# Kernel tuning notes

Measured on AMD Instinct MI355X. Metric: run time of the kernel, lower is better.

The kernel has to match this reference:

```python
import jax, jax.numpy as jnp
import numpy as np

D_MODEL = 1024
N_HEADS = 16
D_HEAD = D_MODEL // N_HEADS
D_FF = 4 * D_MODEL
EPS = 1e-5


def _layernorm(x, g, b):
    mu = jnp.mean(x, axis=-1, keepdims=True)
    var = jnp.var(x, axis=-1, keepdims=True)
    return (x - mu) * jax.lax.rsqrt(var + EPS) * g + b


def setup_inputs() -> dict:
    key = jax.random.key(0)
    ks = jax.random.split(key, 16)
    s_attn = 1.0 / np.sqrt(D_MODEL)
    s_ff1 = 1.0 / np.sqrt(D_MODEL)
    s_ff2 = 1.0 / np.sqrt(D_FF)
    inp = {
        'x': jax.random.normal(ks[0], (2, 2048, D_MODEL), dtype=jnp.float32),
        'Wq': jax.random.uniform(ks[1], (D_MODEL, D_MODEL), jnp.float32, -s_attn, s_attn),
        'bq': jax.random.uniform(ks[2], (D_MODEL,), jnp.float32, -s_attn, s_attn),
        'Wk': jax.random.uniform(ks[3], (D_MODEL, D_MODEL), jnp.float32, -s_attn, s_attn),
        'bk': jax.random.uniform(ks[4], (D_MODEL,), jnp.float32, -s_attn, s_attn),
        'Wv': jax.random.uniform(ks[5], (D_MODEL, D_MODEL), jnp.float32, -s_attn, s_attn),
        'bv': jax.random.uniform(ks[6], (D_MODEL,), jnp.float32, -s_attn, s_attn),
        'Wo': jax.random.uniform(ks[7], (D_MODEL, D_MODEL), jnp.float32, -s_attn, s_attn),
        'bo': jax.random.uniform(ks[8], (D_MODEL,), jnp.float32, -s_attn, s_attn),
        'W1': jax.random.uniform(ks[9], (D_MODEL, D_FF), jnp.float32, -s_ff1, s_ff1),
        'b1': jax.random.uniform(ks[10], (D_FF,), jnp.float32, -s_ff1, s_ff1),
        'W2': jax.random.uniform(ks[11], (D_FF, D_MODEL), jnp.float32, -s_ff2, s_ff2),
        'b2': jax.random.uniform(ks[12], (D_MODEL,), jnp.float32, -s_ff2, s_ff2),
        'ln1_g': jnp.ones((D_MODEL,), jnp.float32),
        'ln1_b': jnp.zeros((D_MODEL,), jnp.float32),
        'ln2_g': jnp.ones((D_MODEL,), jnp.float32),
        'ln2_b': jnp.zeros((D_MODEL,), jnp.float32),
    }
    return inp


def reference(x, Wq, bq, Wk, bk, Wv, bv, Wo, bo, W1, b1, W2, b2, ln1_g, ln1_b, ln2_g, ln2_b):
    B, T, D = x.shape
    scale = D_HEAD ** -0.5

    # pre-norm MHSA + residual
    h = _layernorm(x, ln1_g, ln1_b)
    def split(z):  # [B,T,D] -> [B,H,T,d_h]
        return z.reshape(B, T, N_HEADS, D_HEAD).transpose(0, 2, 1, 3)
    Q = split(h @ Wq + bq)
    K = split(h @ Wk + bk)
    V = split(h @ Wv + bv)
    scores = jnp.einsum('bhqd,bhkd->bhqk', Q, K) * scale  # [B,H,T,T]
    attn = jax.nn.softmax(scores, axis=-1)
    out = jnp.einsum('bhqk,bhkd->bhqd', attn, V)
    out = out.transpose(0, 2, 1, 3).reshape(B, T, D)
    x = x + (out @ Wo + bo)

    # pre-norm FFN + residual
    h = _layernorm(x, ln2_g, ln2_b)
    ff = jax.nn.gelu(h @ W1 + b1, approximate=False) @ W2 + b2
    return x + ff
```

## Files before the change

### kernel.cpp

```cpp
#include <hip/hip_runtime.h>
#include <math.h>

#define SEQ   2048
#define DM    1024
#define LDQKV 3072
#define MTOK  4096

typedef float  f32x4   __attribute__((ext_vector_type(4)));
typedef __bf16 bf16x8  __attribute__((ext_vector_type(8)));
typedef short  short8  __attribute__((ext_vector_type(8)));
typedef short  short4v __attribute__((ext_vector_type(4)));

__device__ __forceinline__ short f2bf(float f) {
  union { float f; unsigned u; } v; v.f = f;
  unsigned r = v.u + 0x7fffu + ((v.u >> 16) & 1u);
  return (short)(r >> 16);
}

__device__ __forceinline__ void gl_lds16(const void* g, void* l) {
  __builtin_amdgcn_global_load_lds(
      (const __attribute__((address_space(1))) void*)g,
      (__attribute__((address_space(3))) void*)l, 16, 0, 0);
}

__device__ __forceinline__ f32x4 mfma_bf16(bf16x8 a, bf16x8 b, f32x4 c) {
  return __builtin_amdgcn_mfma_f32_16x16x32_bf16(a, b, c, 0, 0, 0);
}

__global__ __launch_bounds__(256) void transpose_cast64_k(
    const float* __restrict__ W, short* __restrict__ Wt, int K, int N)
{
  __shared__ float tile[64][65];
  const int n0 = blockIdx.x * 64, k0 = blockIdx.y * 64;
  const int tid = threadIdx.x;
  const int lr = tid >> 4, lc = (tid & 15) * 4;
#pragma unroll
  for (int i = 0; i < 4; i++) {
    const float4 v = *(const float4*)&W[(size_t)(k0 + lr + i * 16) * N + n0 + lc];
    tile[lr + i * 16][lc]     = v.x;
    tile[lr + i * 16][lc + 1] = v.y;
    tile[lr + i * 16][lc + 2] = v.z;
    tile[lr + i * 16][lc + 3] = v.w;
  }
  __syncthreads();
  const int nr = tid >> 3, ks = (tid & 7) * 8;
#pragma unroll
  for (int i = 0; i < 2; i++) {
    short8 o;
#pragma unroll
    for (int j = 0; j < 8; j++) o[j] = f2bf(tile[ks + j][nr + i * 32]);
    *(short8*)&Wt[(size_t)(n0 + nr + i * 32) * K + k0 + ks] = o;
  }
}

__global__ __launch_bounds__(256) void ln_k(
    const float* __restrict__ x, const float* __restrict__ g,
    const float* __restrict__ b, short* __restrict__ out)
{
  const int row = blockIdx.x;
  const int tid = threadIdx.x;
  const float4 v = ((const float4*)(x + (size_t)row * DM))[tid];
  float s  = v.x + v.y + v.z + v.w;
  float ss = v.x * v.x + v.y * v.y + v.z * v.z + v.w * v.w;
#pragma unroll
  for (int m = 32; m >= 1; m >>= 1) { s += __shfl_xor(s, m); ss += __shfl_xor(ss, m); }
  __shared__ float red[8];
  const int wid = tid >> 6;
  if ((tid & 63) == 0) { red[wid] = s; red[4 + wid] = ss; }
  __syncthreads();
  s  = red[0] + red[1] + red[2] + red[3];
  ss = red[4] + red[5] + red[6] + red[7];
  const float mu  = s * (1.f / DM);
  const float var = ss * (1.f / DM) - mu * mu;
  const float rs  = rsqrtf(var + 1e-5f);
  const float4 gv = ((const float4*)g)[tid];
  const float4 bv = ((const float4*)b)[tid];
  short4v o;
  o[0] = f2bf((v.x - mu) * rs * gv.x + bv.x);
  o[1] = f2bf((v.y - mu) * rs * gv.y + bv.y);
  o[2] = f2bf((v.z - mu) * rs * gv.z + bv.z);
  o[3] = f2bf((v.w - mu) * rs * gv.w + bv.w);
  *(short4v*)(out + (size_t)row * DM + tid * 4) = o;
}

__global__ __launch_bounds__(256) void concat_bias_k(
    const float* __restrict__ bq, const float* __restrict__ bk,
    const float* __restrict__ bv, float* __restrict__ o)
{
  int i = blockIdx.x * 256 + threadIdx.x;
  if (i < 3072) {
    float v = (i < 1024) ? bq[i] : (i < 2048 ? bk[i - 1024] : bv[i - 2048]);
    o[i] = v;
  }
}

__global__ __launch_bounds__(256) void vtrans_k(
    const short* __restrict__ V, short* __restrict__ Vt)
{
  const int b = blockIdx.z, h = blockIdx.y, t0 = blockIdx.x * 64;
  __shared__ short tile[64][72];
  const int tid = threadIdx.x;
  const int r = tid >> 2, c = (tid & 3) * 16;
  const short* src = V + (size_t)(b * SEQ + t0 + r) * LDQKV + h * 64 + c;
  *(short8*)&tile[r][c]     = *(const short8*)src;
  *(short8*)&tile[r][c + 8] = *(const short8*)(src + 8);
  __syncthreads();
  const int d = tid >> 2;
  short8 o0, o1;
#pragma unroll
  for (int k = 0; k < 8; k++) o0[k] = tile[c + k][d];
#pragma unroll
  for (int k = 0; k < 8; k++) o1[k] = tile[c + 8 + k][d];
  short* dst = Vt + (((size_t)(b * 16 + h) * 64) + d) * 2048 + t0 + c;
  *(short8*)dst       = o0;
  *(short8*)(dst + 8) = o1;
}

template <bool GELU_, bool RESID, bool OUTBF16>
__global__ __launch_bounds__(512) void gemm256(
    const short* __restrict__ A, const short* __restrict__ Bt,
    const float* __restrict__ bias, const float* __restrict__ resid,
    void* __restrict__ Cout, int M, int N, int K)
{
  __shared__ __align__(16) short Atile[2][256 * 64];
  __shared__ __align__(16) short Btile[2][256 * 64];

  const int tid = threadIdx.x, lane = tid & 63, wid = tid >> 6;
  const int wm = wid >> 2, wn = wid & 3;

  const int nbn = N >> 8;
  const int chunk = gridDim.x >> 3;
  const int swz = (blockIdx.x & 7) * chunk + (blockIdx.x >> 3);
  const int bm = (swz / nbn) * 256;
  const int bn = (swz % nbn) * 256;

  f32x4 acc[8][4] = {};

  const int srow  = wid * 8 + (lane >> 3);
  const int sslot = (lane & 7) ^ ((lane >> 3) & 7);
  const short* Asrc = A  + (size_t)(bm + srow) * K + sslot * 8;
  const short* Bsrc = Bt + (size_t)(bn + srow) * K + sslot * 8;

#define STAGE256(buf, k0)                                                     \
  {                                                                           \
    _Pragma("unroll")                                                         \
    for (int j = 0; j < 4; j++) {                                             \
      gl_lds16(Asrc + (size_t)(j * 64) * K + (k0), &Atile[buf][(j * 64 + wid * 8) * 64]); \
      gl_lds16(Bsrc + (size_t)(j * 64) * K + (k0), &Btile[buf][(j * 64 + wid * 8) * 64]); \
    }                                                                         \
  }

  const int aRowBase = (wm * 128 + (lane & 15)) * 128;
  const int bRowBase = (wn * 64  + (lane & 15)) * 128;
  const int slot0 = (((lane >> 4)    ) ^ (lane & 7)) * 16;
  const int slot1 = (((lane >> 4) + 4) ^ (lane & 7)) * 16;

#define COMPUTE256(buf)                                                       \
  {                                                                           \
    const char* Ab_ = (const char*)&Atile[buf][0];                            \
    const char* Bb_ = (const char*)&Btile[buf][0];                            \
    _Pragma("unroll")                                                         \
    for (int ks = 0; ks < 2; ks++) {                                          \
      const int sl = ks ? slot1 : slot0;                                      \
      bf16x8 a[8], b[4];                                                      \
      _Pragma("unroll")                                                       \
      for (int mi = 0; mi < 8; mi++)                                          \
        a[mi] = *(const bf16x8*)(Ab_ + aRowBase + mi * 2048 + sl);            \
      _Pragma("unroll")                                                       \
      for (int ni = 0; ni < 4; ni++)                                          \
        b[ni] = *(const bf16x8*)(Bb_ + bRowBase + ni * 2048 + sl);            \
      __builtin_amdgcn_s_setprio(1);                                          \
      _Pragma("unroll")                                                       \
      for (int mi = 0; mi < 8; mi++)                                          \
        _Pragma("unroll")                                                     \
        for (int ni = 0; ni < 4; ni++)                                        \
          acc[mi][ni] = mfma_bf16(a[mi], b[ni], acc[mi][ni]);                 \
      __builtin_amdgcn_s_setprio(0);                                          \
    }                                                                         \
  }

  STAGE256(0, 0);
  __syncthreads();

  int cur = 0;
  const int ntiles = K >> 6;
  for (int t = 1; t < ntiles; ++t) {
    STAGE256(cur ^ 1, t * 64);
    COMPUTE256(cur);
    __syncthreads();
    cur ^= 1;
  }
  COMPUTE256(cur);

#pragma unroll
  for (int mi = 0; mi < 8; mi++) {
#pragma unroll
    for (int ni = 0; ni < 4; ni++) {
      const int col = bn + wn * 64 + ni * 16 + (lane & 15);
      const float bs = bias[col];
#pragma unroll
      for (int j = 0; j < 4; j++) {
        const int row = bm + wm * 128 + mi * 16 + (lane >> 4) * 4 + j;
        float v = acc[mi][ni][j] + bs;
        if (GELU_) v = 0.5f * v * (1.0f + erff(v * 0.70710678118654752f));
        if (RESID) v += resid[(size_t)row * N + col];
        if (OUTBF16) ((short*)Cout)[(size_t)row * N + col] = f2bf(v);
        else         ((float*)Cout)[(size_t)row * N + col] = v;
      }
    }
  }
#undef STAGE256
#undef COMPUTE256
}

template <bool GELU_, bool RESID, bool OUTBF16>
__global__ __launch_bounds__(512) void gemm_bt8(
    const short* __restrict__ A, const short* __restrict__ Bt,
    const float* __restrict__ bias, const float* __restrict__ resid,
    void* __restrict__ Cout, int M, int N, int K)
{
  __shared__ __align__(16) short Ab[2][2][128 * 32];
  __shared__ __align__(16) short Bb[2][2][64 * 32];
  const int tid = threadIdx.x, lane = tid & 63, wid = tid >> 6;
  const int kg = wid >> 2, w2 = wid & 3;
  const int wr = w2 >> 1, wc = w2 & 1;
  const int bm = blockIdx.x * 128, bn = blockIdx.y * 64;

  f32x4 acc[4][2] = {};

  const int r_l = lane >> 2;
  const int c8  = ((lane & 3) ^ ((lane >> 2) & 3)) * 8;
  const short* Ag0 = A  + (size_t)(bm + w2 * 32 + r_l)      * K + c8;
  const short* Ag1 = A  + (size_t)(bm + w2 * 32 + 16 + r_l) * K + c8;
  const short* Bg0 = Bt + (size_t)(bn + w2 * 16 + r_l)      * K + c8;

  const int la0 = (w2 * 32) * 32, la1 = (w2 * 32 + 16) * 32, lb0 = (w2 * 16) * 32;
  const int kbase = kg * 32;
  const int rslot = ((lane >> 4) ^ (lane & 3)) * 8;

  gl_lds16(Ag0 + kbase, &Ab[kg][0][la0]);
  gl_lds16(Ag1 + kbase, &Ab[kg][0][la1]);
  gl_lds16(Bg0 + kbase, &Bb[kg][0][lb0]);
  __syncthreads();

  const int nsteps = K >> 6;
  int cur = 0;
  for (int i = 1; i < nsteps; ++i) {
    const int k0 = i * 64 + kbase;
    const int nxt = cur ^ 1;
    gl_lds16(Ag0 + k0, &Ab[kg][nxt][la0]);
    gl_lds16(Ag1 + k0, &Ab[kg][nxt][la1]);
    gl_lds16(Bg0 + k0, &Bb[kg][nxt][lb0]);

    bf16x8 a[4], b[2];
#pragma unroll
    for (int mi = 0; mi < 4; mi++)
      a[mi] = *(const bf16x8*)&Ab[kg][cur][(wr * 64 + mi * 16 + (lane & 15)) * 32 + rslot];
#pragma unroll
    for (int ni = 0; ni < 2; ni++)
      b[ni] = *(const bf16x8*)&Bb[kg][cur][(wc * 32 + ni * 16 + (lane & 15)) * 32 + rslot];
#pragma unroll
    for (int mi = 0; mi < 4; mi++)
#pragma unroll
      for (int ni = 0; ni < 2; ni++)
        acc[mi][ni] = mfma_bf16(a[mi], b[ni], acc[mi][ni]);

    __syncthreads();
    cur = nxt;
  }

  {
    bf16x8 a[4], b[2];
#pragma unroll
    for (int mi = 0; mi < 4; mi++)
      a[mi] = *(const bf16x8*)&Ab[kg][cur][(wr * 64 + mi * 16 + (lane & 15)) * 32 + rslot];
#pragma unroll
    for (int ni = 0; ni < 2; ni++)
      b[ni] = *(const bf16x8*)&Bb[kg][cur][(wc * 32 + ni * 16 + (lane & 15)) * 32 + rslot];
#pragma unroll
    for (int mi = 0; mi < 4; mi++)
#pragma unroll
      for (int ni = 0; ni < 2; ni++)
        acc[mi][ni] = mfma_bf16(a[mi], b[ni], acc[mi][ni]);
  }

  __syncthreads();

  float* red = (float*)&Ab[0][0][0];
  const int slot = (w2 * 64 + lane) * 8;
  if (kg == 1) {
#pragma unroll
    for (int mi = 0; mi < 4; mi++)
#pragma unroll
      for (int ni = 0; ni < 2; ni++)
        *(f32x4*)&red[(slot + mi * 2 + ni) * 4] = acc[mi][ni];
  }
  __syncthreads();
  if (kg == 0) {
#pragma unroll
    for (int mi = 0; mi < 4; mi++)
#pragma unroll
      for (int ni = 0; ni < 2; ni++)
        acc[mi][ni] += *(const f32x4*)&red[(slot + mi * 2 + ni) * 4];

#pragma unroll
    for (int mi = 0; mi < 4; mi++) {
#pragma unroll
      for (int ni = 0; ni < 2; ni++) {
        const int col = bn + wc * 32 + ni * 16 + (lane & 15);
        const float bs = bias[col];
#pragma unroll
        for (int j = 0; j < 4; j++) {
          const int row = bm + wr * 64 + mi * 16 + (lane >> 4) * 4 + j;
          float v = acc[mi][ni][j] + bs;
          if (GELU_) v = 0.5f * v * (1.0f + erff(v * 0.70710678118654752f));
          if (RESID) v += resid[(size_t)row * N + col];
          if (OUTBF16) ((short*)Cout)[(size_t)row * N + col] = f2bf(v);
          else         ((float*)Cout)[(size_t)row * N + col] = v;
        }
      }
    }
  }
}

__global__ __launch_bounds__(512, 4) void attn_k(
    const short* __restrict__ Qg, const short* __restrict__ Kg,
    const short* __restrict__ Vt, short* __restrict__ Og)
{
  const int phys = blockIdx.x;
  const int lg = (phys & 7) * 64 + (phys >> 3);
  const int q0 = (lg & 15) * 128;
  const int h  = (lg >> 4) & 15;
  const int b  = lg >> 8;

  const int tid = threadIdx.x, lane = tid & 63, w = tid >> 6;
  const int qlane = lane & 15, g = lane >> 4;

  __shared__ __align__(16) short Kl[2][128 * 64];
  __shared__ __align__(16) short Vl[2][64 * 128];

  const size_t qrow = (size_t)(b * SEQ + q0 + w * 16 + qlane) * LDQKV + h * 64;
  const bf16x8 qf0 = *(const bf16x8*)&Qg[qrow + g * 8];
  const bf16x8 qf1 = *(const bf16x8*)&Qg[qrow + 32 + g * 8];

  const int kslot = (lane & 7) ^ ((lane >> 3) & 7);
  const short* Kg_a[2];
#pragma unroll
  for (int i = 0; i < 2; i++) {
    const int r  = i * 64 + w * 8 + (lane >> 3);
    const int kc = r >> 4, gr = (r >> 2) & 3, jr = r & 3;
    const int a  = 32 * (kc & 3) + 8 * gr + 4 * (kc >> 2) + jr;
    Kg_a[i] = Kg + ((size_t)(b * SEQ) + a) * LDQKV + h * 64 + kslot * 8;
  }
  const short* Vg_s[2];
#pragma unroll
  for (int i = 0; i < 2; i++) {
    const int d  = i * 32 + w * 4 + (lane >> 4);
    const int vs = (lane & 15) ^ (d & 15);
    Vg_s[i] = Vt + ((size_t)(b * 16 + h) * 64 + d) * 2048 + vs * 8;
  }

  float m_run = -1e30f, l_run = 0.f;
  f32x4 oacc[4] = {};
  const float C = 0.125f * 1.44269504088896f;

#pragma unroll
  for (int i = 0; i < 2; i++) {
    gl_lds16(Kg_a[i], &Kl[0][(i * 64 + w * 8) * 64]);
    gl_lds16(Vg_s[i], &Vl[0][(i * 32 + w * 4) * 128]);
  }
  __syncthreads();

  int cur = 0;
  for (int kt = 0; kt < SEQ; kt += 128) {
    const int nxt = cur ^ 1;
    if (kt + 128 < SEQ) {
#pragma unroll
      for (int i = 0; i < 2; i++) {
        gl_lds16(Kg_a[i] + (size_t)(kt + 128) * LDQKV, &Kl[nxt][(i * 64 + w * 8) * 64]);
        gl_lds16(Vg_s[i] + (kt + 128),                 &Vl[nxt][(i * 32 + w * 4) * 128]);
      }
    }
    const char* KbC = (const char*)&Kl[cur][0];
    const char* VbC = (const char*)&Vl[cur][0];

    f32x4 s[8];
#pragma unroll
    for (int kc = 0; kc < 8; kc++) {
      const int kr = kc * 16 + qlane;
      const char* kp = KbC + kr * 128;
      const int sw = (kr & 7) << 4;
      bf16x8 kf0 = *(const bf16x8*)(kp + ((g * 16) ^ sw));
      bf16x8 kf1 = *(const bf16x8*)(kp + ((64 + g * 16) ^ sw));
      f32x4 z = {};
      z = mfma_bf16(kf0, qf0, z);
      z = mfma_bf16(kf1, qf1, z);
      s[kc] = z;
    }

    f32x4 m4 = s[0];
#pragma unroll
    for (int kc = 1; kc < 8; kc++) {
      m4[0] = fmaxf(m4[0], s[kc][0]); m4[1] = fmaxf(m4[1], s[kc][1]);
      m4[2] = fmaxf(m4[2], s[kc][2]); m4[3] = fmaxf(m4[3], s[kc][3]);
    }
    float mt = fmaxf(fmaxf(m4[0], m4[1]), fmaxf(m4[2], m4[3]));
    mt = fmaxf(mt, __shfl_xor(mt, 16));
    mt = fmaxf(mt, __shfl_xor(mt, 32));

    if (!__all(mt - m_run <= 40.0f)) {
      const float mnew = fmaxf(m_run, mt);
      const float r = exp2f((m_run - mnew) * C);
      m_run = mnew;
      l_run *= r;
#pragma unroll
      for (int j = 0; j < 4; j++) {
        const float rj = __shfl(r, g * 4 + j);
#pragma unroll
        for (int dt = 0; dt < 4; dt++) oacc[dt][j] *= rj;
      }
    }

    const float nmc = -m_run * C;
    float rs = 0.f;
    unsigned pw[4][4];
#pragma unroll
    for (int kc = 0; kc < 8; kc++) {
      f32x4 p;
#pragma unroll
      for (int j = 0; j < 4; j++) p[j] = exp2f(fmaf(s[kc][j], C, nmc));
      rs += (p[0] + p[1]) + (p[2] + p[3]);
      unsigned w0, w1;
      asm("v_cvt_pk_bf16_f32 %0, %1, %2" : "=v"(w0) : "v"(p[0]), "v"(p[1]));
      asm("v_cvt_pk_bf16_f32 %0, %1, %2" : "=v"(w1) : "v"(p[2]), "v"(p[3]));
      pw[kc & 3][2 * (kc >> 2) + 0] = w0;
      pw[kc & 3][2 * (kc >> 2) + 1] = w1;
    }
    rs += __shfl_xor(rs, 16);
    rs += __shfl_xor(rs, 32);
    l_run += rs;

#pragma unroll
    for (int ks = 0; ks < 4; ks++) {
      union { unsigned u[4]; bf16x8 v; } pf;
      pf.u[0] = pw[ks][0]; pf.u[1] = pw[ks][1];
      pf.u[2] = pw[ks][2]; pf.u[3] = pw[ks][3];
#pragma unroll
      for (int dt = 0; dt < 4; dt++) {
        const int vr = dt * 16 + qlane;
        bf16x8 vf = *(const bf16x8*)(VbC + vr * 256 + ((64 * ks + 16 * g) ^ ((vr & 15) << 4)));
        oacc[dt] = mfma_bf16(pf.v, vf, oacc[dt]);
      }
    }

    __syncthreads();
    cur = nxt;
  }

  const float linv = 1.f / l_run;
#pragma unroll
  for (int j = 0; j < 4; j++) {
    const float lj = __shfl(linv, g * 4 + j);
    const int tok = q0 + w * 16 + g * 4 + j;
#pragma unroll
    for (int dt = 0; dt < 4; dt++)
      Og[(size_t)(b * SEQ + tok) * DM + h * 64 + dt * 16 + qlane] = f2bf(oacc[dt][j] * lj);
  }
}

extern "C" void kernel_launch(void* const* d_in, const int* in_sizes, int n_in,
                              void* d_out, int out_size, void* d_ws, size_t ws_size,
                              hipStream_t stream)
{
  const float* x    = (const float*)d_in[0];
  const float* Wq   = (const float*)d_in[1];
  const float* bq   = (const float*)d_in[2];
  const float* Wk   = (const float*)d_in[3];
  const float* bk   = (const float*)d_in[4];
  const float* Wv   = (const float*)d_in[5];
  const float* bv   = (const float*)d_in[6];
  const float* Wo   = (const float*)d_in[7];
  const float* bo   = (const float*)d_in[8];
  const float* W1   = (const float*)d_in[9];
  const float* b1   = (const float*)d_in[10];
  const float* W2   = (const float*)d_in[11];
  const float* b2   = (const float*)d_in[12];
  const float* ln1g = (const float*)d_in[13];
  const float* ln1b = (const float*)d_in[14];
  const float* ln2g = (const float*)d_in[15];
  const float* ln2b = (const float*)d_in[16];

  char* ws = (char*)d_ws;
  const size_t MB = 1024 * 1024;
  short* Wqkvt = (short*)(ws + 0 * MB);
  short* Wqt   = Wqkvt;
  short* Wkt   = (short*)(ws + 2 * MB);
  short* Wvt   = (short*)(ws + 4 * MB);
  short* Wot   = (short*)(ws + 6 * MB);
  short* W1t   = (short*)(ws + 8 * MB);
  short* W2t   = (short*)(ws + 16 * MB);
  short* hbuf  = (short*)(ws + 24 * MB);
  short* QKV   = (short*)(ws + 32 * MB);
  short* AO    = (short*)(ws + 56 * MB);
  float* x1    = (float*)(ws + 64 * MB);
  short* Vtb   = (short*)(ws + 64 * MB);
  float* bqkv  = (float*)(ws + 80 * MB);
  short* gbuf  = (short*)(ws + 32 * MB);

  dim3 tb(256);

  transpose_cast64_k<<<dim3(16, 16), tb, 0, stream>>>(Wq, Wqt, 1024, 1024);
  transpose_cast64_k<<<dim3(16, 16), tb, 0, stream>>>(Wk, Wkt, 1024, 1024);
  transpose_cast64_k<<<dim3(16, 16), tb, 0, stream>>>(Wv, Wvt, 1024, 1024);
  transpose_cast64_k<<<dim3(16, 16), tb, 0, stream>>>(Wo, Wot, 1024, 1024);
  transpose_cast64_k<<<dim3(64, 16), tb, 0, stream>>>(W1, W1t, 1024, 4096);
  transpose_cast64_k<<<dim3(16, 64), tb, 0, stream>>>(W2, W2t, 4096, 1024);
  concat_bias_k<<<dim3(12), tb, 0, stream>>>(bq, bk, bv, bqkv);

  ln_k<<<dim3(MTOK), tb, 0, stream>>>(x, ln1g, ln1b, hbuf);

  gemm256<false, false, true><<<dim3(192), dim3(512), 0, stream>>>(
      hbuf, Wqkvt, bqkv, nullptr, QKV, MTOK, 3072, 1024);

  vtrans_k<<<dim3(32, 16, 2), tb, 0, stream>>>(QKV + 2048, Vtb);

  attn_k<<<dim3(512), dim3(512), 0, stream>>>(QKV, QKV + 1024, Vtb, AO);

  gemm_bt8<false, true, false><<<dim3(32, 16), dim3(512), 0, stream>>>(
      AO, Wot, bo, x, x1, MTOK, 1024, 1024);

  ln_k<<<dim3(MTOK), tb, 0, stream>>>(x1, ln2g, ln2b, hbuf);

  gemm256<true, false, true><<<dim3(256), dim3(512), 0, stream>>>(
      hbuf, W1t, b1, nullptr, gbuf, MTOK, 4096, 1024);

  gemm_bt8<false, true, false><<<dim3(32, 16), dim3(512), 0, stream>>>(
      gbuf, W2t, b2, x1, (float*)d_out, MTOK, 1024, 4096);
}
```

Measured before the change: 272.4 us.

## Triple-buffer GEMM K-loop with partial vmcnt waits and reswizzled LDS layout

Both GEMM kernels move from double-buffered LDS staging with full __syncthreads to a three-stage ring. Each loop iteration now waits with s_waitcnt vmcnt only for the oldest outstanding tile, so two tiles of global-to-LDS loads stay in flight during compute. The 256x256 kernel also halves its K-tile to 32, which changes the swizzle and staging pattern and roughly halves its LDS footprint. The gain sought is better overlap of memory latency; the cost is twice as many barriers per K in gemm256 and added LDS use in gemm_bt8, which may reduce occupancy.

```diff
diff --git a/kernel.cpp b/kernel.cpp
--- a/kernel.cpp
+++ b/kernel.cpp
@@ -122,8 +122,8 @@
     const float* __restrict__ bias, const float* __restrict__ resid,
     void* __restrict__ Cout, int M, int N, int K)
 {
-  __shared__ __align__(16) short Atile[2][256 * 64];
-  __shared__ __align__(16) short Btile[2][256 * 64];
+  __shared__ __align__(16) short Atile[3][256 * 32];
+  __shared__ __align__(16) short Btile[3][256 * 32];
 
   const int tid = threadIdx.x, lane = tid & 63, wid = tid >> 6;
   const int wm = wid >> 2, wn = wid & 3;
@@ -136,61 +136,61 @@
 
   f32x4 acc[8][4] = {};
 
-  const int srow  = wid * 8 + (lane >> 3);
-  const int sslot = (lane & 7) ^ ((lane >> 3) & 7);
-  const short* Asrc = A  + (size_t)(bm + srow) * K + sslot * 8;
-  const short* Bsrc = Bt + (size_t)(bn + srow) * K + sslot * 8;
+  const int srow = tid >> 2;
+  const int scol = ((tid & 3) ^ ((srow >> 1) & 3)) * 8;
+  const short* Asrc = A  + (size_t)(bm + srow) * K + scol;
+  const short* Bsrc = Bt + (size_t)(bn + srow) * K + scol;
+  const int dst0 = (wid * 16) * 32, dst1 = (128 + wid * 16) * 32;
 
 #define STAGE256(buf, k0)                                                     \
   {                                                                           \
-    _Pragma("unroll")                                                         \
-    for (int j = 0; j < 4; j++) {                                             \
-      gl_lds16(Asrc + (size_t)(j * 64) * K + (k0), &Atile[buf][(j * 64 + wid * 8) * 64]); \
-      gl_lds16(Bsrc + (size_t)(j * 64) * K + (k0), &Btile[buf][(j * 64 + wid * 8) * 64]); \
-    }                                                                         \
-  }
-
-  const int aRowBase = (wm * 128 + (lane & 15)) * 128;
-  const int bRowBase = (wn * 64  + (lane & 15)) * 128;
-  const int slot0 = (((lane >> 4)    ) ^ (lane & 7)) * 16;
-  const int slot1 = (((lane >> 4) + 4) ^ (lane & 7)) * 16;
+    gl_lds16(Asrc + (k0),                   &Atile[buf][dst0]);               \
+    gl_lds16(Asrc + (size_t)128 * K + (k0), &Atile[buf][dst1]);               \
+    gl_lds16(Bsrc + (k0),                   &Btile[buf][dst0]);               \
+    gl_lds16(Bsrc + (size_t)128 * K + (k0), &Btile[buf][dst1]);               \
+  }
+
+  const int rrow  = lane & 15;
+  const int rslot = (((lane >> 4) ^ ((rrow >> 1) & 3))) * 8;
+  const int aOff  = (wm * 128 + rrow) * 32 + rslot;
+  const int bOff  = (wn * 64  + rrow) * 32 + rslot;
 
 #define COMPUTE256(buf)                                                       \
   {                                                                           \
-    const char* Ab_ = (const char*)&Atile[buf][0];                            \
-    const char* Bb_ = (const char*)&Btile[buf][0];                            \
+    const short* Ab_ = &Atile[buf][0];                                        \
+    const short* Bb_ = &Btile[buf][0];                                        \
+    bf16x8 a[8], b[4];                                                        \
     _Pragma("unroll")                                                         \
-    for (int ks = 0; ks < 2; ks++) {                                          \
-      const int sl = ks ? slot1 : slot0;                                      \
-      bf16x8 a[8], b[4];                                                      \
-      _Pragma("unroll")                                                       \
-      for (int mi = 0; mi < 8; mi++)                                          \
-        a[mi] = *(const bf16x8*)(Ab_ + aRowBase + mi * 2048 + sl);            \
+    for (int mi = 0; mi < 8; mi++)                                            \
+      a[mi] = *(const bf16x8*)(Ab_ + aOff + mi * 512);                        \
+    _Pragma("unroll")                                                         \
+    for (int ni = 0; ni < 4; ni++)                                            \
+      b[ni] = *(const bf16x8*)(Bb_ + bOff + ni * 512);                        \
+    __builtin_amdgcn_s_setprio(1);                                            \
+    _Pragma("unroll")                                                         \
+    for (int mi = 0; mi < 8; mi++)                                            \
       _Pragma("unroll")                                                       \
       for (int ni = 0; ni < 4; ni++)                                          \
-        b[ni] = *(const bf16x8*)(Bb_ + bRowBase + ni * 2048 + sl);            \
-      __builtin_amdgcn_s_setprio(1);                                          \
-      _Pragma("unroll")                                                       \
-      for (int mi = 0; mi < 8; mi++)                                          \
-        _Pragma("unroll")                                                     \
-        for (int ni = 0; ni < 4; ni++)                                        \
-          acc[mi][ni] = mfma_bf16(a[mi], b[ni], acc[mi][ni]);                 \
-      __builtin_amdgcn_s_setprio(0);                                          \
-    }                                                                         \
-  }
-
+        acc[mi][ni] = mfma_bf16(a[mi], b[ni], acc[mi][ni]);                   \
+    __builtin_amdgcn_s_setprio(0);                                            \
+  }
+
+  const int ntiles = K >> 5;
   STAGE256(0, 0);
-  __syncthreads();
-
-  int cur = 0;
-  const int ntiles = K >> 6;
-  for (int t = 1; t < ntiles; ++t) {
-    STAGE256(cur ^ 1, t * 64);
-    COMPUTE256(cur);
-    __syncthreads();
-    cur ^= 1;
-  }
-  COMPUTE256(cur);
+  STAGE256(1, 32);
+  asm volatile("s_waitcnt vmcnt(4)" ::: "memory");
+  __builtin_amdgcn_s_barrier();
+
+  int bufc = 0;
+  for (int t = 0; t < ntiles; ++t) {
+    const int b2 = (bufc + 2 >= 3) ? bufc - 1 : bufc + 2;
+    if (t + 2 < ntiles) STAGE256(b2, (t + 2) * 32);
+    COMPUTE256(bufc);
+    if (t + 2 < ntiles)      { asm volatile("s_waitcnt vmcnt(4)" ::: "memory"); }
+    else if (t + 1 < ntiles) { asm volatile("s_waitcnt vmcnt(0)" ::: "memory"); }
+    __builtin_amdgcn_s_barrier();
+    bufc = (bufc + 1 == 3) ? 0 : bufc + 1;
+  }
 
 #pragma unroll
   for (int mi = 0; mi < 8; mi++) {
@@ -219,8 +219,8 @@
     const float* __restrict__ bias, const float* __restrict__ resid,
     void* __restrict__ Cout, int M, int N, int K)
 {
-  __shared__ __align__(16) short Ab[2][2][128 * 32];
-  __shared__ __align__(16) short Bb[2][2][64 * 32];
+  __shared__ __align__(16) short Ab[2][3][128 * 32];
+  __shared__ __align__(16) short Bb[2][3][64 * 32];
   const int tid = threadIdx.x, lane = tid & 63, wid = tid >> 6;
   const int kg = wid >> 2, w2 = wid & 3;
   const int wr = w2 >> 1, wc = w2 & 1;
@@ -229,59 +229,55 @@
   f32x4 acc[4][2] = {};
 
   const int r_l = lane >> 2;
-  const int c8  = ((lane & 3) ^ ((lane >> 2) & 3)) * 8;
+  const int c8  = ((lane & 3) ^ ((lane >> 3) & 3)) * 8;
   const short* Ag0 = A  + (size_t)(bm + w2 * 32 + r_l)      * K + c8;
   const short* Ag1 = A  + (size_t)(bm + w2 * 32 + 16 + r_l) * K + c8;
   const short* Bg0 = Bt + (size_t)(bn + w2 * 16 + r_l)      * K + c8;
 
   const int la0 = (w2 * 32) * 32, la1 = (w2 * 32 + 16) * 32, lb0 = (w2 * 16) * 32;
   const int kbase = kg * 32;
-  const int rslot = ((lane >> 4) ^ (lane & 3)) * 8;
-
-  gl_lds16(Ag0 + kbase, &Ab[kg][0][la0]);
-  gl_lds16(Ag1 + kbase, &Ab[kg][0][la1]);
-  gl_lds16(Bg0 + kbase, &Bb[kg][0][lb0]);
-  __syncthreads();
+  const int rslot = ((lane >> 4) ^ ((lane >> 1) & 3)) * 8;
+
+#define STAGE8(buf, k0)                                                       \
+  {                                                                           \
+    gl_lds16(Ag0 + (k0), &Ab[kg][buf][la0]);                                  \
+    gl_lds16(Ag1 + (k0), &Ab[kg][buf][la1]);                                  \
+    gl_lds16(Bg0 + (k0), &Bb[kg][buf][lb0]);                                  \
+  }
+
+#define COMPUTE8(buf)                                                         \
+  {                                                                           \
+    bf16x8 a[4], b[2];                                                        \
+    _Pragma("unroll")                                                         \
+    for (int mi = 0; mi < 4; mi++)                                            \
+      a[mi] = *(const bf16x8*)&Ab[kg][buf][(wr * 64 + mi * 16 + (lane & 15)) * 32 + rslot]; \
+    _Pragma("unroll")                                                         \
+    for (int ni = 0; ni < 2; ni++)                                            \
+      b[ni] = *(const bf16x8*)&Bb[kg][buf][(wc * 32 + ni * 16 + (lane & 15)) * 32 + rslot]; \
+    __builtin_amdgcn_s_setprio(1);                                            \
+    _Pragma("unroll")                                                         \
+    for (int mi = 0; mi < 4; mi++)                                            \
+      _Pragma("unroll")                                                       \
+      for (int ni = 0; ni < 2; ni++)                                          \
+        acc[mi][ni] = mfma_bf16(a[mi], b[ni], acc[mi][ni]);                   \
+    __builtin_amdgcn_s_setprio(0);                                            \
+  }
 
   const int nsteps = K >> 6;
-  int cur = 0;
-  for (int i = 1; i < nsteps; ++i) {
-    const int k0 = i * 64 + kbase;
-    const int nxt = cur ^ 1;
-    gl_lds16(Ag0 + k0, &Ab[kg][nxt][la0]);
-    gl_lds16(Ag1 + k0, &Ab[kg][nxt][la1]);
-    gl_lds16(Bg0 + k0, &Bb[kg][nxt][lb0]);
-
-    bf16x8 a[4], b[2];
-#pragma unroll
-    for (int mi = 0; mi < 4; mi++)
-      a[mi] = *(const bf16x8*)&Ab[kg][cur][(wr * 64 + mi * 16 + (lane & 15)) * 32 + rslot];
-#pragma unroll
-    for (int ni = 0; ni < 2; ni++)
-      b[ni] = *(const bf16x8*)&Bb[kg][cur][(wc * 32 + ni * 16 + (lane & 15)) * 32 + rslot];
-#pragma unroll
-    for (int mi = 0; mi < 4; mi++)
-#pragma unroll
-      for (int ni = 0; ni < 2; ni++)
-        acc[mi][ni] = mfma_bf16(a[mi], b[ni], acc[mi][ni]);
-
-    __syncthreads();
-    cur = nxt;
-  }
-
-  {
-    bf16x8 a[4], b[2];
-#pragma unroll
-    for (int mi = 0; mi < 4; mi++)
-      a[mi] = *(const bf16x8*)&Ab[kg][cur][(wr * 64 + mi * 16 + (lane & 15)) * 32 + rslot];
-#pragma unroll
-    for (int ni = 0; ni < 2; ni++)
-      b[ni] = *(const bf16x8*)&Bb[kg][cur][(wc * 32 + ni * 16 + (lane & 15)) * 32 + rslot];
-#pragma unroll
-    for (int mi = 0; mi < 4; mi++)
-#pragma unroll
-      for (int ni = 0; ni < 2; ni++)
-        acc[mi][ni] = mfma_bf16(a[mi], b[ni], acc[mi][ni]);
+  STAGE8(0, kbase);
+  STAGE8(1, 64 + kbase);
+  asm volatile("s_waitcnt vmcnt(3)" ::: "memory");
+  __builtin_amdgcn_s_barrier();
+
+  int bufc = 0;
+  for (int i = 0; i < nsteps; ++i) {
+    const int b2 = (bufc + 2 >= 3) ? bufc - 1 : bufc + 2;
+    if (i + 2 < nsteps) STAGE8(b2, (i + 2) * 64 + kbase);
+    COMPUTE8(bufc);
+    if (i + 2 < nsteps)      { asm volatile("s_waitcnt vmcnt(3)" ::: "memory"); }
+    else if (i + 1 < nsteps) { asm volatile("s_waitcnt vmcnt(0)" ::: "memory"); }
+    __builtin_amdgcn_s_barrier();
+    bufc = (bufc + 1 == 3) ? 0 : bufc + 1;
   }
 
   __syncthreads();
@@ -321,6 +317,8 @@
       }
     }
   }
+#undef STAGE8
+#undef COMPUTE8
 }
 
 __global__ __launch_bounds__(512, 4) void attn_k(
```

New measurement: 285.9 us. 1.05x slower.
